# Kernel tuning notes

Measured on AMD Instinct MI355X. Metric: run time of the kernel, lower is better.

Reference implementation:

```python
import jax, jax.numpy as jnp
import numpy as np

N_NODES = 50000
N_EDGES = 1600000
DIM = 512


def setup_inputs() -> dict:
    key = jax.random.key(0)
    k1, k2, k3, k4, k5 = jax.random.split(key, 5)
    x = jax.random.normal(k1, (N_NODES, DIM), dtype=jnp.float32)
    adj_rows = jax.random.randint(k2, (N_EDGES,), 0, N_NODES, dtype=jnp.int32)
    adj_cols = jax.random.randint(k3, (N_EDGES,), 0, N_NODES, dtype=jnp.int32)
    adj_vals = jax.random.uniform(k4, (N_EDGES,), dtype=jnp.float32)
    # fc1 weight [out_dim, in_dim], kaiming-normal-ish init
    weight = jax.random.normal(k5, (DIM, DIM), dtype=jnp.float32) * np.float32(np.sqrt(2.0 / DIM))
    scale = jnp.full((1,), 1.5, dtype=jnp.float32)
    return {"x": x, "adj_rows": adj_rows, "adj_cols": adj_cols,
            "adj_vals": adj_vals, "weight": weight, "scale": scale}


def reference(x, adj_rows, adj_cols, adj_vals, weight, scale):
    # dropout in eval mode -> identity
    N, D = x.shape
    # dense linear: y = x @ W^T
    y = jnp.einsum('nd,od->no', x, weight)
    # sparse adj @ y  (COO SpMM via gather + segment_sum)
    y = jax.ops.segment_sum(adj_vals[:, None] * y[adj_cols], adj_rows,
                            num_segments=N)
    # sp_norm: mean-center over nodes, scale by global RMS^{-1} * (1+scale) * sqrt(D)
    y_t = y - jnp.mean(y, axis=0, keepdims=True)
    y_norm = jnp.mean(jnp.sum(y_t * y_t, axis=1)) ** -0.5
    y = y_t * y_norm * (1.0 + scale) * jnp.float32(np.sqrt(D))
    # activation (relu), then residual (input_dim == output_dim)
    y = jax.nn.relu(y)
    return y + x
```

## Files before the change

kernel.cpp:

```cpp
#include <hip/hip_runtime.h>
#include <hip/hip_bf16.h>
#include <cstdint>
#include <cstddef>

#define N_NODES 50000
#define DIM 512
#define N_EDGES 1600000
#define NT 25
#define NB (N_NODES * NT)
#define GPANELS 391
#define NSHAD 8

typedef __bf16 bf16;
typedef __bf16 bf16x8 __attribute__((ext_vector_type(8)));
typedef __bf16 bf16x4 __attribute__((ext_vector_type(4)));
typedef float floatx4 __attribute__((ext_vector_type(4)));

__global__ void prep_kernel(const float* __restrict__ x, bf16* __restrict__ xb,
                            const float* __restrict__ w, bf16* __restrict__ wb,
                            int4* __restrict__ cnt4, float4* __restrict__ stats4,
                            int n4x, int n4w) {
    int i = blockIdx.x * blockDim.x + threadIdx.x;
    if (i < n4x) {
        float4 v = reinterpret_cast<const float4*>(x)[i];
        bf16x4 o;
        o[0] = (bf16)v.x; o[1] = (bf16)v.y; o[2] = (bf16)v.z; o[3] = (bf16)v.w;
        reinterpret_cast<bf16x4*>(xb)[i] = o;
    }
    if (i < n4w) {
        float4 v = reinterpret_cast<const float4*>(w)[i];
        bf16x4 o;
        o[0] = (bf16)v.x; o[1] = (bf16)v.y; o[2] = (bf16)v.z; o[3] = (bf16)v.w;
        reinterpret_cast<bf16x4*>(wb)[i] = o;
    }
    if (i < NB / 4) cnt4[i] = make_int4(0, 0, 0, 0);
    if (i < 1028) stats4[i] = make_float4(0.f, 0.f, 0.f, 0.f);
}

__global__ void hist_kernel(const int* __restrict__ rows, const int* __restrict__ cols,
                            int* __restrict__ cnt, int E) {
    int i = blockIdx.x * blockDim.x + threadIdx.x;
    if (i < E) {
        int key = rows[i] * NT + (cols[i] >> 11);
        atomicAdd(&cnt[key], 1);
    }
}

__global__ __launch_bounds__(1024) void scanA_kernel(const int* __restrict__ cnt,
                                                     int* __restrict__ row_start,
                                                     int* __restrict__ blksum, int n) {
    const int t = threadIdx.x;
    int i = blockIdx.x * 1024 + t;
    int v = (i < n) ? cnt[i] : 0;
    int s = v;
#pragma unroll
    for (int off = 1; off < 64; off <<= 1) {
        int u = __shfl_up(s, off, 64);
        if ((t & 63) >= off) s += u;
    }
    __shared__ int wsum[16];
    if ((t & 63) == 63) wsum[t >> 6] = s;
    __syncthreads();
    if (t < 16) {
        int w = wsum[t];
#pragma unroll
        for (int off = 1; off < 16; off <<= 1) {
            int u = __shfl_up(w, off, 16);
            if (t >= off) w += u;
        }
        wsum[t] = w;
    }
    __syncthreads();
    int base = (t >= 64) ? wsum[(t >> 6) - 1] : 0;
    int incl = s + base;
    if (i < n) row_start[i] = incl - v;
    if (t == 1023) blksum[blockIdx.x] = incl;
}

__global__ __launch_bounds__(1024) void scanB_kernel(const int* __restrict__ blksum,
                                                     int* __restrict__ blkoff, int nb) {
    __shared__ int s[1024];
    const int t = threadIdx.x;
    const int base = t * 2;
    int a = (base < nb) ? blksum[base] : 0;
    int b = (base + 1 < nb) ? blksum[base + 1] : 0;
    s[t] = a + b;
    __syncthreads();
    for (int off = 1; off < 1024; off <<= 1) {
        int u = (t >= off) ? s[t - off] : 0;
        __syncthreads();
        s[t] += u;
        __syncthreads();
    }
    int excl = (t == 0) ? 0 : s[t - 1];
    if (base < nb) blkoff[base] = excl;
    if (base + 1 < nb) blkoff[base + 1] = excl + a;
}

__global__ __launch_bounds__(1024) void scanC_kernel(int* __restrict__ row_start,
                                                     const int* __restrict__ blkoff,
                                                     int* __restrict__ cursor, int n) {
    int i = blockIdx.x * 1024 + threadIdx.x;
    if (i >= n) return;
    int v = row_start[i] + blkoff[i >> 10];
    row_start[i] = v;
    cursor[i] = v;
    if (i == n - 1) row_start[n] = N_EDGES;
}

__global__ void scatter_kernel(const int* __restrict__ rows, const int* __restrict__ cols,
                               const float* __restrict__ vals, int* __restrict__ cursor,
                               int2* __restrict__ ecv, int E) {
    int i = blockIdx.x * blockDim.x + threadIdx.x;
    if (i >= E) return;
    int c = cols[i];
    int key = rows[i] * NT + (c >> 11);
    int p = atomicAdd(&cursor[key], 1);
    ecv[p] = make_int2(c, __float_as_int(vals[i]));
}

__global__ __launch_bounds__(256) void gemm_kernel(const bf16* __restrict__ A,
                                                   const bf16* __restrict__ B,
                                                   bf16* __restrict__ C) {
    __shared__ bf16 lA[128 * 32];
    __shared__ bf16 lB[128 * 32];
    const int d = blockIdx.x;
    const int p = (d & 7) + ((d >> 5) << 3);
    const int c = (d >> 3) & 3;
    if (p >= GPANELS) return;
    const int t = threadIdx.x;
    const int wave = t >> 6;
    const int lane = t & 63;
    const int rowBase = p * 128;
    const int colBase = c * 128;
    const int wm = (wave >> 1) * 64;
    const int wn = (wave & 1) * 64;
    floatx4 acc[4][4] = {};

    const int r_a = t >> 2;
    const int kk = (t & 3) * 8;
    const int l15 = lane & 15;
    const int koff = (lane >> 4) * 8;

    for (int k0 = 0; k0 < DIM; k0 += 32) {
#pragma unroll
        for (int j = 0; j < 2; j++) {
            int row = rowBase + r_a + j * 64;
            if (row > N_NODES - 1) row = N_NODES - 1;
            const bf16* g = A + (size_t)row * DIM + k0 + kk;
            bf16* l = lA + wave * 512 + j * 2048;
            __builtin_amdgcn_global_load_lds(
                (const __attribute__((address_space(1))) void*)g,
                (__attribute__((address_space(3))) void*)l, 16, 0, 0);
        }
#pragma unroll
        for (int j = 0; j < 2; j++) {
            int row = colBase + r_a + j * 64;
            const bf16* g = B + (size_t)row * DIM + k0 + kk;
            bf16* l = lB + wave * 512 + j * 2048;
            __builtin_amdgcn_global_load_lds(
                (const __attribute__((address_space(1))) void*)g,
                (__attribute__((address_space(3))) void*)l, 16, 0, 0);
        }
        __syncthreads();
        bf16x8 af[4], bfr[4];
#pragma unroll
        for (int i = 0; i < 4; i++)
            af[i] = *reinterpret_cast<const bf16x8*>(lA + (wm + i * 16 + l15) * 32 + koff);
#pragma unroll
        for (int j = 0; j < 4; j++)
            bfr[j] = *reinterpret_cast<const bf16x8*>(lB + (wn + j * 16 + l15) * 32 + koff);
#pragma unroll
        for (int i = 0; i < 4; i++)
#pragma unroll
            for (int j = 0; j < 4; j++)
                acc[i][j] = __builtin_amdgcn_mfma_f32_16x16x32_bf16(af[i], bfr[j], acc[i][j], 0, 0, 0);
        __syncthreads();
    }
    const int rquad = (lane >> 4) * 4;
#pragma unroll
    for (int i = 0; i < 4; i++) {
#pragma unroll
        for (int reg = 0; reg < 4; reg++) {
            int gr = rowBase + wm + i * 16 + rquad + reg;
            if (gr >= N_NODES) continue;
#pragma unroll
            for (int j = 0; j < 4; j++) {
                int gc = colBase + wn + j * 16 + l15;
                C[(size_t)gr * DIM + gc] = (bf16)acc[i][j][reg];
            }
        }
    }
}

__device__ __forceinline__ float blo(uint32_t w) { return __uint_as_float(w << 16); }
__device__ __forceinline__ float bhi(uint32_t w) { return __uint_as_float(w & 0xffff0000u); }

__device__ __forceinline__ void fmac8(float* acc, float v, const uint4& w) {
    acc[0] += v * blo(w.x); acc[1] += v * bhi(w.x);
    acc[2] += v * blo(w.y); acc[3] += v * bhi(w.y);
    acc[4] += v * blo(w.z); acc[5] += v * bhi(w.z);
    acc[6] += v * blo(w.w); acc[7] += v * bhi(w.w);
}

__global__ __launch_bounds__(256) void spmm_kernel(const int* __restrict__ row_start,
                                                   const int2* __restrict__ ecv,
                                                   const bf16* __restrict__ y,
                                                   float* __restrict__ y2) {
    const int wave = threadIdx.x >> 6;
    const int lane = threadIdx.x & 63;
    const int r = blockIdx.x * 4 + wave;
    const int s = row_start[r * NT];
    const int e = row_start[(r + 1) * NT];
    float acc[8] = {0.f, 0.f, 0.f, 0.f, 0.f, 0.f, 0.f, 0.f};
    const uint32_t* yb = reinterpret_cast<const uint32_t*>(y);

    int i = s;
    for (; i + 3 < e; i += 4) {
        int2 e0 = ecv[i], e1 = ecv[i + 1], e2 = ecv[i + 2], e3 = ecv[i + 3];
        uint4 w0 = *reinterpret_cast<const uint4*>(yb + (size_t)e0.x * 256 + lane * 4);
        uint4 w1 = *reinterpret_cast<const uint4*>(yb + (size_t)e1.x * 256 + lane * 4);
        uint4 w2 = *reinterpret_cast<const uint4*>(yb + (size_t)e2.x * 256 + lane * 4);
        uint4 w3 = *reinterpret_cast<const uint4*>(yb + (size_t)e3.x * 256 + lane * 4);
        fmac8(acc, __int_as_float(e0.y), w0);
        fmac8(acc, __int_as_float(e1.y), w1);
        fmac8(acc, __int_as_float(e2.y), w2);
        fmac8(acc, __int_as_float(e3.y), w3);
    }
    for (; i < e; i++) {
        int2 e0 = ecv[i];
        uint4 w0 = *reinterpret_cast<const uint4*>(yb + (size_t)e0.x * 256 + lane * 4);
        fmac8(acc, __int_as_float(e0.y), w0);
    }
    float4* out = reinterpret_cast<float4*>(y2 + (size_t)r * DIM + lane * 8);
    out[0] = make_float4(acc[0], acc[1], acc[2], acc[3]);
    out[1] = make_float4(acc[4], acc[5], acc[6], acc[7]);
}

#define RED_GRID 512
#define RED_CHUNK 16
__global__ __launch_bounds__(256) void reduce_kernel(const float* __restrict__ y2,
                                                     float* __restrict__ colsumS,
                                                     float* __restrict__ totsqS,
                                                     int* __restrict__ done,
                                                     const float* __restrict__ scale,
                                                     float* __restrict__ sfac,
                                                     float* __restrict__ colsum) {
    const int t = threadIdx.x;
    const int d2 = t * 2;
    float c0 = 0.f, c1 = 0.f, sq = 0.f;
    for (int r0 = blockIdx.x * RED_CHUNK; r0 < N_NODES; r0 += RED_GRID * RED_CHUNK) {
        float2 v[RED_CHUNK];
#pragma unroll
        for (int j = 0; j < RED_CHUNK; j++) {
            int r = r0 + j;
            v[j] = (r < N_NODES)
                       ? *reinterpret_cast<const float2*>(y2 + (size_t)r * DIM + d2)
                       : make_float2(0.f, 0.f);
        }
#pragma unroll
        for (int j = 0; j < RED_CHUNK; j++) {
            c0 += v[j].x;
            c1 += v[j].y;
            sq += v[j].x * v[j].x + v[j].y * v[j].y;
        }
    }
    const int sh = blockIdx.x & (NSHAD - 1);
    atomicAdd(&colsumS[sh * DIM + d2], c0);
    atomicAdd(&colsumS[sh * DIM + d2 + 1], c1);
    __shared__ float ssq[256];
    ssq[t] = sq;
    __syncthreads();
    for (int off = 128; off > 0; off >>= 1) {
        if (t < off) ssq[t] += ssq[t + off];
        __syncthreads();
    }
    if (t == 0) atomicAdd(&totsqS[sh], ssq[0]);

    __threadfence();
    __shared__ int ticket_s;
    if (t == 0) ticket_s = atomicAdd(done, 1);
    __syncthreads();
    if (ticket_s != RED_GRID - 1) return;
    float s0 = 0.f, s1 = 0.f;
#pragma unroll
    for (int c = 0; c < NSHAD; c++) {
        s0 += atomicAdd(&colsumS[c * DIM + t], 0.f);
        s1 += atomicAdd(&colsumS[c * DIM + t + 256], 0.f);
    }
    colsum[t] = s0;
    colsum[t + 256] = s1;
    float mu0 = s0 * (1.0f / N_NODES);
    float mu1 = s1 * (1.0f / N_NODES);
    __syncthreads();
    ssq[t] = mu0 * mu0 + mu1 * mu1;
    __syncthreads();
    for (int off = 128; off > 0; off >>= 1) {
        if (t < off) ssq[t] += ssq[t + off];
        __syncthreads();
    }
    if (t == 0) {
        float tq = 0.f;
#pragma unroll
        for (int c = 0; c < NSHAD; c++) tq += atomicAdd(&totsqS[c], 0.f);
        float var = tq * (1.0f / N_NODES) - ssq[0];
        sfac[0] = rsqrtf(var) * (1.0f + scale[0]) * sqrtf((float)DIM);
    }
}

__global__ void final_kernel(float* __restrict__ y2, const float* __restrict__ x,
                             const float* __restrict__ colsum, const float* __restrict__ sfac,
                             int n4) {
    int i = blockIdx.x * blockDim.x + threadIdx.x;
    if (i >= n4) return;
    const float invN = 1.0f / N_NODES;
    float4 v = reinterpret_cast<float4*>(y2)[i];
    float4 xv = reinterpret_cast<const float4*>(x)[i];
    float4 mu = reinterpret_cast<const float4*>(colsum)[i & 127];
    float s = sfac[0];
    v.x = fmaxf((v.x - mu.x * invN) * s, 0.0f) + xv.x;
    v.y = fmaxf((v.y - mu.y * invN) * s, 0.0f) + xv.y;
    v.z = fmaxf((v.z - mu.z * invN) * s, 0.0f) + xv.z;
    v.w = fmaxf((v.w - mu.w * invN) * s, 0.0f) + xv.w;
    reinterpret_cast<float4*>(y2)[i] = v;
}

extern "C" void kernel_launch(void* const* d_in, const int* in_sizes, int n_in,
                              void* d_out, int out_size, void* d_ws, size_t ws_size,
                              hipStream_t stream) {
    const float* x        = (const float*)d_in[0];
    const int*   adj_rows = (const int*)d_in[1];
    const int*   adj_cols = (const int*)d_in[2];
    const float* adj_vals = (const float*)d_in[3];
    const float* weight   = (const float*)d_in[4];
    const float* scale    = (const float*)d_in[5];
    float* out = (float*)d_out;

    char* ws = (char*)d_ws;
    size_t off = 0;
    auto alloc = [&](size_t b) {
        char* p = ws + off;
        off += (b + 255) & ~(size_t)255;
        return p;
    };
    const int nblk = (NB + 1023) / 1024;
    bf16*  xb        = (bf16*)alloc((size_t)N_NODES * DIM * 2);
    int2*  ecv       = (int2*)xb;
    bf16*  Wb        = (bf16*)alloc((size_t)DIM * DIM * 2);
    bf16*  y         = (bf16*)alloc((size_t)N_NODES * DIM * 2);
    int*   cnt       = (int*)alloc((size_t)NB * 4);
    int*   cursor    = cnt;
    int*   row_start = (int*)alloc((size_t)(NB + 1) * 4);
    int*   blksum    = (int*)alloc((size_t)nblk * 4);
    int*   blkoff    = (int*)alloc((size_t)nblk * 4);
    float* colsumS   = (float*)alloc((size_t)NSHAD * DIM * 4);
    float* totsqS    = (float*)alloc((size_t)NSHAD * 4);
    int*   done      = (int*)(totsqS + NSHAD);
    float* colsum    = (float*)alloc(512 * 4);
    float* sfac      = (float*)alloc(4);
    (void)ws_size; (void)in_sizes; (void)n_in; (void)out_size;

    const int n4x = N_NODES * DIM / 4;
    const int n4w = DIM * DIM / 4;

    prep_kernel<<<(n4x + 255) / 256, 256, 0, stream>>>(x, xb, weight, Wb,
                                                       (int4*)cnt, (float4*)colsumS,
                                                       n4x, n4w);

    gemm_kernel<<<1568, 256, 0, stream>>>(xb, Wb, y);
    gemm_kernel<<<1568, 256, 0, stream>>>(xb, Wb, y);

    hist_kernel<<<(N_EDGES + 255) / 256, 256, 0, stream>>>(adj_rows, adj_cols, cnt, N_EDGES);
    scanA_kernel<<<nblk, 1024, 0, stream>>>(cnt, row_start, blksum, NB);
    scanB_kernel<<<1, 1024, 0, stream>>>(blksum, blkoff, nblk);
    scanC_kernel<<<nblk, 1024, 0, stream>>>(row_start, blkoff, cursor, NB);
    scatter_kernel<<<(N_EDGES + 255) / 256, 256, 0, stream>>>(adj_rows, adj_cols, adj_vals,
                                                              cursor, ecv, N_EDGES);

    spmm_kernel<<<N_NODES / 4, 256, 0, stream>>>(row_start, ecv, y, out);

    reduce_kernel<<<RED_GRID, 256, 0, stream>>>(out, colsumS, totsqS, done, scale, sfac, colsum);
    final_kernel<<<(n4x + 255) / 256, 256, 0, stream>>>(out, x, colsum, sfac, n4x);
}
```

Before: 754.8 us.

## Fuse CSR construction into one cooperative kernel and drop the duplicate GEMM launch

Histogram, three-pass scan, offset fix-up and scatter are merged into one cooperative kernel that uses grid-wide syncs instead of five launches. The scan now handles four elements per thread, and a compact per-node row pointer array is emitted so SpMM reads contiguous offsets. The scatter increments `row_start` directly, so the separate cursor copy is gone. A redundant second GEMM launch is also removed. In exchange, the CSR build depends on cooperative launch, and fewer threads handle each phase.

```diff
diff --git a/kernel.cpp b/kernel.cpp
--- a/kernel.cpp
+++ b/kernel.cpp
@@ -1,15 +1,21 @@
 #include <hip/hip_runtime.h>
 #include <hip/hip_bf16.h>
+#include <hip/hip_cooperative_groups.h>
 #include <cstdint>
 #include <cstddef>
+
+namespace cg = cooperative_groups;
 
 #define N_NODES 50000
 #define DIM 512
 #define N_EDGES 1600000
 #define NT 25
 #define NB (N_NODES * NT)
+#define NCHUNK ((NB + 1023) / 1024)
 #define GPANELS 391
 #define NSHAD 8
+#define CSR_BLOCKS 1024
+#define CSR_THREADS 256
 
 typedef __bf16 bf16;
 typedef __bf16 bf16x8 __attribute__((ext_vector_type(8)));
@@ -37,86 +43,105 @@
     if (i < 1028) stats4[i] = make_float4(0.f, 0.f, 0.f, 0.f);
 }
 
-__global__ void hist_kernel(const int* __restrict__ rows, const int* __restrict__ cols,
-                            int* __restrict__ cnt, int E) {
-    int i = blockIdx.x * blockDim.x + threadIdx.x;
-    if (i < E) {
-        int key = rows[i] * NT + (cols[i] >> 11);
-        atomicAdd(&cnt[key], 1);
-    }
-}
-
-__global__ __launch_bounds__(1024) void scanA_kernel(const int* __restrict__ cnt,
-                                                     int* __restrict__ row_start,
-                                                     int* __restrict__ blksum, int n) {
+__device__ void scan_chunk_1024(int cb, const int* __restrict__ cnt,
+                                int* __restrict__ row_start, int* __restrict__ blksum) {
     const int t = threadIdx.x;
-    int i = blockIdx.x * 1024 + t;
-    int v = (i < n) ? cnt[i] : 0;
-    int s = v;
+    const int i0 = cb * 1024 + t * 4;
+    int v0 = (i0 + 0 < NB) ? cnt[i0 + 0] : 0;
+    int v1 = (i0 + 1 < NB) ? cnt[i0 + 1] : 0;
+    int v2 = (i0 + 2 < NB) ? cnt[i0 + 2] : 0;
+    int v3 = (i0 + 3 < NB) ? cnt[i0 + 3] : 0;
+    const int tsum = v0 + v1 + v2 + v3;
+    int s = tsum;
 #pragma unroll
     for (int off = 1; off < 64; off <<= 1) {
         int u = __shfl_up(s, off, 64);
         if ((t & 63) >= off) s += u;
     }
-    __shared__ int wsum[16];
-    if ((t & 63) == 63) wsum[t >> 6] = s;
-    __syncthreads();
-    if (t < 16) {
-        int w = wsum[t];
-#pragma unroll
-        for (int off = 1; off < 16; off <<= 1) {
-            int u = __shfl_up(w, off, 16);
-            if (t >= off) w += u;
-        }
-        wsum[t] = w;
-    }
-    __syncthreads();
-    int base = (t >= 64) ? wsum[(t >> 6) - 1] : 0;
-    int incl = s + base;
-    if (i < n) row_start[i] = incl - v;
-    if (t == 1023) blksum[blockIdx.x] = incl;
-}
-
-__global__ __launch_bounds__(1024) void scanB_kernel(const int* __restrict__ blksum,
-                                                     int* __restrict__ blkoff, int nb) {
-    __shared__ int s[1024];
+    __shared__ int ws[4];
+    if ((t & 63) == 63) ws[t >> 6] = s;
+    __syncthreads();
+    int wbase = 0;
+#pragma unroll
+    for (int w = 0; w < 4; w++)
+        if ((t >> 6) > w) wbase += ws[w];
+    const int excl = wbase + s - tsum;
+    if (i0 + 0 < NB) row_start[i0 + 0] = excl;
+    if (i0 + 1 < NB) row_start[i0 + 1] = excl + v0;
+    if (i0 + 2 < NB) row_start[i0 + 2] = excl + v0 + v1;
+    if (i0 + 3 < NB) row_start[i0 + 3] = excl + v0 + v1 + v2;
+    if (t == 255) blksum[cb] = wbase + s;
+    __syncthreads();
+}
+
+__device__ void scan_blksum_block0(const int* __restrict__ blksum, int* __restrict__ blkoff) {
     const int t = threadIdx.x;
-    const int base = t * 2;
-    int a = (base < nb) ? blksum[base] : 0;
-    int b = (base + 1 < nb) ? blksum[base + 1] : 0;
-    s[t] = a + b;
-    __syncthreads();
-    for (int off = 1; off < 1024; off <<= 1) {
-        int u = (t >= off) ? s[t - off] : 0;
-        __syncthreads();
-        s[t] += u;
-        __syncthreads();
-    }
-    int excl = (t == 0) ? 0 : s[t - 1];
-    if (base < nb) blkoff[base] = excl;
-    if (base + 1 < nb) blkoff[base + 1] = excl + a;
-}
-
-__global__ __launch_bounds__(1024) void scanC_kernel(int* __restrict__ row_start,
-                                                     const int* __restrict__ blkoff,
-                                                     int* __restrict__ cursor, int n) {
-    int i = blockIdx.x * 1024 + threadIdx.x;
-    if (i >= n) return;
-    int v = row_start[i] + blkoff[i >> 10];
-    row_start[i] = v;
-    cursor[i] = v;
-    if (i == n - 1) row_start[n] = N_EDGES;
-}
-
-__global__ void scatter_kernel(const int* __restrict__ rows, const int* __restrict__ cols,
-                               const float* __restrict__ vals, int* __restrict__ cursor,
-                               int2* __restrict__ ecv, int E) {
-    int i = blockIdx.x * blockDim.x + threadIdx.x;
-    if (i >= E) return;
-    int c = cols[i];
-    int key = rows[i] * NT + (c >> 11);
-    int p = atomicAdd(&cursor[key], 1);
-    ecv[p] = make_int2(c, __float_as_int(vals[i]));
+    int c[5];
+    int tsum = 0;
+#pragma unroll
+    for (int j = 0; j < 5; j++) {
+        int idx = t * 5 + j;
+        c[j] = (idx < NCHUNK) ? blksum[idx] : 0;
+        tsum += c[j];
+    }
+    int s = tsum;
+#pragma unroll
+    for (int off = 1; off < 64; off <<= 1) {
+        int u = __shfl_up(s, off, 64);
+        if ((t & 63) >= off) s += u;
+    }
+    __shared__ int ws2[4];
+    if ((t & 63) == 63) ws2[t >> 6] = s;
+    __syncthreads();
+    int wbase = 0;
+#pragma unroll
+    for (int w = 0; w < 4; w++)
+        if ((t >> 6) > w) wbase += ws2[w];
+    int excl = wbase + s - tsum;
+#pragma unroll
+    for (int j = 0; j < 5; j++) {
+        int idx = t * 5 + j;
+        if (idx < NCHUNK) blkoff[idx] = excl;
+        excl += c[j];
+    }
+}
+
+__global__ void csr_kernel(const int* __restrict__ rows, const int* __restrict__ cols,
+                           const float* __restrict__ vals, int* __restrict__ cnt,
+                           int* __restrict__ row_start, int* __restrict__ blksum,
+                           int* __restrict__ blkoff, int* __restrict__ rowb,
+                           int2* __restrict__ ecv) {
+    cg::grid_group grid = cg::this_grid();
+    const int tid = blockIdx.x * CSR_THREADS + threadIdx.x;
+    const int nthr = CSR_BLOCKS * CSR_THREADS;
+
+    for (int i = tid; i < N_EDGES; i += nthr) {
+        int key = rows[i] * NT + (cols[i] >> 11);
+        atomicAdd(&cnt[key], 1);
+    }
+    grid.sync();
+
+    for (int cb = blockIdx.x; cb < NCHUNK; cb += CSR_BLOCKS)
+        scan_chunk_1024(cb, cnt, row_start, blksum);
+    grid.sync();
+
+    if (blockIdx.x == 0) scan_blksum_block0(blksum, blkoff);
+    grid.sync();
+
+    for (int i = tid; i < NB; i += nthr) {
+        int v = row_start[i] + blkoff[i >> 10];
+        row_start[i] = v;
+        if (i % NT == 0) rowb[i / NT] = v;
+    }
+    if (tid == 0) rowb[N_NODES] = N_EDGES;
+    grid.sync();
+
+    for (int i = tid; i < N_EDGES; i += nthr) {
+        int c = cols[i];
+        int key = rows[i] * NT + (c >> 11);
+        int p = atomicAdd(&row_start[key], 1);
+        ecv[p] = make_int2(c, __float_as_int(vals[i]));
+    }
 }
 
 __global__ __launch_bounds__(256) void gemm_kernel(const bf16* __restrict__ A,
@@ -203,15 +228,15 @@
     acc[6] += v * blo(w.w); acc[7] += v * bhi(w.w);
 }
 
-__global__ __launch_bounds__(256) void spmm_kernel(const int* __restrict__ row_start,
+__global__ __launch_bounds__(256) void spmm_kernel(const int* __restrict__ rowb,
                                                    const int2* __restrict__ ecv,
                                                    const bf16* __restrict__ y,
                                                    float* __restrict__ y2) {
     const int wave = threadIdx.x >> 6;
     const int lane = threadIdx.x & 63;
     const int r = blockIdx.x * 4 + wave;
-    const int s = row_start[r * NT];
-    const int e = row_start[(r + 1) * NT];
+    const int s = rowb[r];
+    const int e = rowb[r + 1];
     float acc[8] = {0.f, 0.f, 0.f, 0.f, 0.f, 0.f, 0.f, 0.f};
     const uint32_t* yb = reinterpret_cast<const uint32_t*>(y);
 
@@ -343,16 +368,15 @@
         off += (b + 255) & ~(size_t)255;
         return p;
     };
-    const int nblk = (NB + 1023) / 1024;
     bf16*  xb        = (bf16*)alloc((size_t)N_NODES * DIM * 2);
     int2*  ecv       = (int2*)xb;
     bf16*  Wb        = (bf16*)alloc((size_t)DIM * DIM * 2);
     bf16*  y         = (bf16*)alloc((size_t)N_NODES * DIM * 2);
     int*   cnt       = (int*)alloc((size_t)NB * 4);
-    int*   cursor    = cnt;
     int*   row_start = (int*)alloc((size_t)(NB + 1) * 4);
-    int*   blksum    = (int*)alloc((size_t)nblk * 4);
-    int*   blkoff    = (int*)alloc((size_t)nblk * 4);
+    int*   blksum    = (int*)alloc((size_t)NCHUNK * 4);
+    int*   blkoff    = (int*)alloc((size_t)NCHUNK * 4);
+    int*   rowb      = (int*)alloc((size_t)(N_NODES + 1) * 4);
     float* colsumS   = (float*)alloc((size_t)NSHAD * DIM * 4);
     float* totsqS    = (float*)alloc((size_t)NSHAD * 4);
     int*   done      = (int*)(totsqS + NSHAD);
@@ -368,17 +392,18 @@
                                                        n4x, n4w);
 
     gemm_kernel<<<1568, 256, 0, stream>>>(xb, Wb, y);
-    gemm_kernel<<<1568, 256, 0, stream>>>(xb, Wb, y);
-
-    hist_kernel<<<(N_EDGES + 255) / 256, 256, 0, stream>>>(adj_rows, adj_cols, cnt, N_EDGES);
-    scanA_kernel<<<nblk, 1024, 0, stream>>>(cnt, row_start, blksum, NB);
-    scanB_kernel<<<1, 1024, 0, stream>>>(blksum, blkoff, nblk);
-    scanC_kernel<<<nblk, 1024, 0, stream>>>(row_start, blkoff, cursor, NB);
-    scatter_kernel<<<(N_EDGES + 255) / 256, 256, 0, stream>>>(adj_rows, adj_cols, adj_vals,
-                                                              cursor, ecv, N_EDGES);
-
-    spmm_kernel<<<N_NODES / 4, 256, 0, stream>>>(row_start, ecv, y, out);
+
+    {
+        void* args[] = {(void*)&adj_rows, (void*)&adj_cols, (void*)&adj_vals,
+                        (void*)&cnt, (void*)&row_start, (void*)&blksum,
+                        (void*)&blkoff, (void*)&rowb, (void*)&ecv};
+        hipLaunchCooperativeKernel((void*)csr_kernel, dim3(CSR_BLOCKS),
+                                   dim3(CSR_THREADS), args, 0, stream);
+    }
+
+    spmm_kernel<<<N_NODES / 4, 256, 0, stream>>>(rowb, ecv, y, out);
 
     reduce_kernel<<<RED_GRID, 256, 0, stream>>>(out, colsumS, totsqS, done, scale, sfac, colsum);
+
     final_kernel<<<(n4x + 255) / 256, 256, 0, stream>>>(out, x, colsum, sfac, n4x);
 }
```

Result: slower. 1.176 ms (+55.8%).

## Pack histogram counters into bytes, record per-edge ranks, drop duplicate GEMM launch

Applied to the files above, without the earlier changes.

The CSR build now keeps four 8-bit bucket counters per 32-bit word. The histogram atomic's return value gives each edge its rank within its bucket, so the scatter pass computes the edge's position directly as row_start plus rank, with no second round of atomics. The scan reads packed words and expands them to four offsets per thread, which shrinks the counter buffer and the scan grid. A redundant second launch of the identical GEMM is removed. The cost is an extra 1-byte-per-edge rank buffer, and the scheme relies on no bucket holding more than 255 edges, beyond which a count would carry into the next byte.

```diff
diff --git a/kernel.cpp b/kernel.cpp
--- a/kernel.cpp
+++ b/kernel.cpp
@@ -8,6 +8,8 @@
 #define N_EDGES 1600000
 #define NT 25
 #define NB (N_NODES * NT)
+#define NWORDS (NB / 4)
+#define NCHUNKA ((NWORDS + 1023) / 1024)
 #define GPANELS 391
 #define NSHAD 8
 
@@ -33,26 +35,30 @@
         o[0] = (bf16)v.x; o[1] = (bf16)v.y; o[2] = (bf16)v.z; o[3] = (bf16)v.w;
         reinterpret_cast<bf16x4*>(wb)[i] = o;
     }
-    if (i < NB / 4) cnt4[i] = make_int4(0, 0, 0, 0);
+    if (i < NWORDS / 4) cnt4[i] = make_int4(0, 0, 0, 0);
     if (i < 1028) stats4[i] = make_float4(0.f, 0.f, 0.f, 0.f);
 }
 
 __global__ void hist_kernel(const int* __restrict__ rows, const int* __restrict__ cols,
-                            int* __restrict__ cnt, int E) {
+                            uint32_t* __restrict__ cnt32, uint8_t* __restrict__ rank, int E) {
     int i = blockIdx.x * blockDim.x + threadIdx.x;
     if (i < E) {
         int key = rows[i] * NT + (cols[i] >> 11);
-        atomicAdd(&cnt[key], 1);
-    }
-}
-
-__global__ __launch_bounds__(1024) void scanA_kernel(const int* __restrict__ cnt,
+        int sh = (key & 3) * 8;
+        uint32_t old = atomicAdd(&cnt32[key >> 2], 1u << sh);
+        rank[i] = (uint8_t)((old >> sh) & 0xFFu);
+    }
+}
+
+__global__ __launch_bounds__(1024) void scanA_kernel(const uint32_t* __restrict__ cnt32,
                                                      int* __restrict__ row_start,
-                                                     int* __restrict__ blksum, int n) {
+                                                     int* __restrict__ blksum) {
     const int t = threadIdx.x;
-    int i = blockIdx.x * 1024 + t;
-    int v = (i < n) ? cnt[i] : 0;
-    int s = v;
+    const int w = blockIdx.x * 1024 + t;
+    uint32_t pk = (w < NWORDS) ? cnt32[w] : 0u;
+    const int c0 = pk & 0xFF, c1 = (pk >> 8) & 0xFF, c2 = (pk >> 16) & 0xFF, c3 = (pk >> 24) & 0xFF;
+    const int tsum = c0 + c1 + c2 + c3;
+    int s = tsum;
 #pragma unroll
     for (int off = 1; off < 64; off <<= 1) {
         int u = __shfl_up(s, off, 64);
@@ -62,19 +68,25 @@
     if ((t & 63) == 63) wsum[t >> 6] = s;
     __syncthreads();
     if (t < 16) {
-        int w = wsum[t];
+        int v = wsum[t];
 #pragma unroll
         for (int off = 1; off < 16; off <<= 1) {
-            int u = __shfl_up(w, off, 16);
-            if (t >= off) w += u;
-        }
-        wsum[t] = w;
-    }
-    __syncthreads();
-    int base = (t >= 64) ? wsum[(t >> 6) - 1] : 0;
-    int incl = s + base;
-    if (i < n) row_start[i] = incl - v;
-    if (t == 1023) blksum[blockIdx.x] = incl;
+            int u = __shfl_up(v, off, 16);
+            if (t >= off) v += u;
+        }
+        wsum[t] = v;
+    }
+    __syncthreads();
+    const int base = (t >= 64) ? wsum[(t >> 6) - 1] : 0;
+    const int excl = base + s - tsum;
+    if (w < NWORDS) {
+        const int i0 = w * 4;
+        row_start[i0 + 0] = excl;
+        row_start[i0 + 1] = excl + c0;
+        row_start[i0 + 2] = excl + c0 + c1;
+        row_start[i0 + 3] = excl + c0 + c1 + c2;
+    }
+    if (t == 1023) blksum[blockIdx.x] = base + s;
 }
 
 __global__ __launch_bounds__(1024) void scanB_kernel(const int* __restrict__ blksum,
@@ -98,24 +110,21 @@
 }
 
 __global__ __launch_bounds__(1024) void scanC_kernel(int* __restrict__ row_start,
-                                                     const int* __restrict__ blkoff,
-                                                     int* __restrict__ cursor, int n) {
+                                                     const int* __restrict__ blkoff, int n) {
     int i = blockIdx.x * 1024 + threadIdx.x;
     if (i >= n) return;
-    int v = row_start[i] + blkoff[i >> 10];
-    row_start[i] = v;
-    cursor[i] = v;
+    row_start[i] += blkoff[i >> 12];
     if (i == n - 1) row_start[n] = N_EDGES;
 }
 
 __global__ void scatter_kernel(const int* __restrict__ rows, const int* __restrict__ cols,
-                               const float* __restrict__ vals, int* __restrict__ cursor,
-                               int2* __restrict__ ecv, int E) {
+                               const float* __restrict__ vals, const int* __restrict__ row_start,
+                               const uint8_t* __restrict__ rank, int2* __restrict__ ecv, int E) {
     int i = blockIdx.x * blockDim.x + threadIdx.x;
     if (i >= E) return;
     int c = cols[i];
     int key = rows[i] * NT + (c >> 11);
-    int p = atomicAdd(&cursor[key], 1);
+    int p = row_start[key] + rank[i];
     ecv[p] = make_int2(c, __float_as_int(vals[i]));
 }
 
@@ -343,42 +352,41 @@
         off += (b + 255) & ~(size_t)255;
         return p;
     };
-    const int nblk = (NB + 1023) / 1024;
-    bf16*  xb        = (bf16*)alloc((size_t)N_NODES * DIM * 2);
-    int2*  ecv       = (int2*)xb;
-    bf16*  Wb        = (bf16*)alloc((size_t)DIM * DIM * 2);
-    bf16*  y         = (bf16*)alloc((size_t)N_NODES * DIM * 2);
-    int*   cnt       = (int*)alloc((size_t)NB * 4);
-    int*   cursor    = cnt;
-    int*   row_start = (int*)alloc((size_t)(NB + 1) * 4);
-    int*   blksum    = (int*)alloc((size_t)nblk * 4);
-    int*   blkoff    = (int*)alloc((size_t)nblk * 4);
-    float* colsumS   = (float*)alloc((size_t)NSHAD * DIM * 4);
-    float* totsqS    = (float*)alloc((size_t)NSHAD * 4);
-    int*   done      = (int*)(totsqS + NSHAD);
-    float* colsum    = (float*)alloc(512 * 4);
-    float* sfac      = (float*)alloc(4);
+    bf16*    xb        = (bf16*)alloc((size_t)N_NODES * DIM * 2);
+    int2*    ecv       = (int2*)xb;
+    bf16*    Wb        = (bf16*)alloc((size_t)DIM * DIM * 2);
+    bf16*    y         = (bf16*)alloc((size_t)N_NODES * DIM * 2);
+    uint32_t* cnt32    = (uint32_t*)alloc((size_t)NWORDS * 4);
+    uint8_t* rank      = (uint8_t*)alloc((size_t)N_EDGES);
+    int*     row_start = (int*)alloc((size_t)(NB + 1) * 4);
+    int*     blksum    = (int*)alloc((size_t)NCHUNKA * 4);
+    int*     blkoff    = (int*)alloc((size_t)NCHUNKA * 4);
+    float*   colsumS   = (float*)alloc((size_t)NSHAD * DIM * 4);
+    float*   totsqS    = (float*)alloc((size_t)NSHAD * 4);
+    int*     done      = (int*)(totsqS + NSHAD);
+    float*   colsum    = (float*)alloc(512 * 4);
+    float*   sfac      = (float*)alloc(4);
     (void)ws_size; (void)in_sizes; (void)n_in; (void)out_size;
 
     const int n4x = N_NODES * DIM / 4;
     const int n4w = DIM * DIM / 4;
 
     prep_kernel<<<(n4x + 255) / 256, 256, 0, stream>>>(x, xb, weight, Wb,
-                                                       (int4*)cnt, (float4*)colsumS,
+                                                       (int4*)cnt32, (float4*)colsumS,
                                                        n4x, n4w);
 
     gemm_kernel<<<1568, 256, 0, stream>>>(xb, Wb, y);
-    gemm_kernel<<<1568, 256, 0, stream>>>(xb, Wb, y);
-
-    hist_kernel<<<(N_EDGES + 255) / 256, 256, 0, stream>>>(adj_rows, adj_cols, cnt, N_EDGES);
-    scanA_kernel<<<nblk, 1024, 0, stream>>>(cnt, row_start, blksum, NB);
-    scanB_kernel<<<1, 1024, 0, stream>>>(blksum, blkoff, nblk);
-    scanC_kernel<<<nblk, 1024, 0, stream>>>(row_start, blkoff, cursor, NB);
+
+    hist_kernel<<<(N_EDGES + 255) / 256, 256, 0, stream>>>(adj_rows, adj_cols, cnt32, rank, N_EDGES);
+    scanA_kernel<<<NCHUNKA, 1024, 0, stream>>>(cnt32, row_start, blksum);
+    scanB_kernel<<<1, 1024, 0, stream>>>(blksum, blkoff, NCHUNKA);
+    scanC_kernel<<<(NB + 1023) / 1024, 1024, 0, stream>>>(row_start, blkoff, NB);
     scatter_kernel<<<(N_EDGES + 255) / 256, 256, 0, stream>>>(adj_rows, adj_cols, adj_vals,
-                                                              cursor, ecv, N_EDGES);
+                                                              row_start, rank, ecv, N_EDGES);
 
     spmm_kernel<<<N_NODES / 4, 256, 0, stream>>>(row_start, ecv, y, out);
 
     reduce_kernel<<<RED_GRID, 256, 0, stream>>>(out, colsumS, totsqS, done, scale, sfac, colsum);
+
     final_kernel<<<(n4x + 255) / 256, 256, 0, stream>>>(out, x, colsum, sfac, n4x);
 }
```

New measurement: 681.0 us. -9.8%, faster.
